# Optimization experiments

Hardware: AMD Instinct MI355X
Metric: run time of the kernel (lower is better)

The kernel has to match this reference:

```python
import jax, jax.numpy as jnp
import numpy as np

B, C_IN, H, W = 2048, 192, 19, 19
G1, P1 = 32, 32

def setup_inputs() -> dict:
    key = jax.random.key(0)
    ks = jax.random.split(key, 10)
    inputs = jax.random.normal(ks[0], (B, C_IN, H, W), dtype=jnp.float32)
    # binary validity mask (most points valid), plus its per-sample sum
    mask = (jax.random.uniform(ks[1], (B, 1, H, W)) > 0.1).astype(jnp.float32)
    mask_sum_hw = jnp.sum(mask, axis=(2, 3), keepdims=True)  # [B,1,1,1]
    s = 0.05
    return {
        "inputs": inputs,
        "mask": mask,
        "mask_sum_hw": mask_sum_hw,
        "w1p": jax.random.normal(ks[2], (P1, C_IN), dtype=jnp.float32) * s,
        "b1p": jnp.zeros((P1,), jnp.float32),
        "w1g": jax.random.normal(ks[3], (G1, C_IN), dtype=jnp.float32) * s,
        "b1g": jnp.zeros((G1,), jnp.float32),
        "beta_g": jnp.zeros((1, G1, 1, 1), jnp.float32),
        "w_lin": jax.random.normal(ks[4], (P1, 3 * G1), dtype=jnp.float32) * s,
        "b_lin": jnp.zeros((P1,), jnp.float32),
        "beta2": jnp.zeros((1, P1, 1, 1), jnp.float32),
        "w2p": jax.random.normal(ks[5], (1, P1), dtype=jnp.float32) * s,
        "b2p": jnp.zeros((1,), jnp.float32),
    }

def _conv1x1(x, w, b):
    # x: [B,C,H,W], w: [O,C] -> [B,O,H,W]
    return jnp.einsum('bchw,oc->bohw', x, w) + b[None, :, None, None]

def _gpool(x, mask, mask_sum_hw):
    # x: [B,G,H,W]; returns [B,3G,1,1]
    off = (jnp.sqrt(mask_sum_hw) - 28.0) / 10.0
    mean = jnp.sum(x, axis=(2, 3), keepdims=True) / mask_sum_hw
    mx = jnp.max(x + (mask - 1.0), axis=(2, 3), keepdims=True)
    return jnp.concatenate([mean, mean * off, mx], axis=1)

def reference(inputs, mask, mask_sum_hw, w1p, b1p, w1g, b1g, beta_g,
              w_lin, b_lin, beta2, w2p, b2p):
    b, _, h, w = inputs.shape
    outp = _conv1x1(inputs, w1p, b1p)                      # [B,P1,H,W]
    outg = _conv1x1(inputs, w1g, b1g)                      # [B,G1,H,W]
    outg = (outg + beta_g) * mask                          # NormMask (no gamma)
    outg = jax.nn.gelu(outg, approximate=False)            # torch GELU = exact erf
    outg = _gpool(outg, mask, mask_sum_hw)                 # [B,3G1,1,1]
    outg = outg.reshape(b, -1) @ w_lin.T + b_lin           # [B,P1]
    outp = outp + outg[:, :, None, None]
    outp = (outp + beta2) * mask                           # NormMask
    outp = jax.nn.gelu(outp, approximate=False)
    outp = _conv1x1(outp, w2p, b2p)                        # [B,1,H,W]
    outp = outp - (1.0 - mask) * 5000.0
    outp = jax.nn.log_softmax(outp.reshape(b, -1), axis=1)
    return outp.reshape(b, h, w)
```

## Files before the change

kernel.cpp:

```cpp
#include <hip/hip_runtime.h>
#include <hip/hip_bf16.h>
#include <math.h>

#define NBLK   256
#define EPB    8
#define CIN    192
#define HW     361
#define NTH    512
#define NSTAGE 48
#define TILE_BYTES 46208
#define SLOTS  2888
#define PSLOTS 3072

typedef float f32x4 __attribute__((ext_vector_type(4)));
typedef short s16x8 __attribute__((ext_vector_type(8)));

__device__ __forceinline__ unsigned short f2bf_bits(float f) {
    __hip_bfloat16 h = __float2bfloat16(f);
    unsigned short s;
    __builtin_memcpy(&s, &h, sizeof(s));
    return s;
}
__device__ __forceinline__ unsigned int packbf(float lo, float hi) {
    return (unsigned int)f2bf_bits(lo) | ((unsigned int)f2bf_bits(hi) << 16);
}

__device__ __forceinline__ float gelu_fast(float x) {
    float inner = x * fmaf(0.044715f, x * x, 1.0f);
    float t = 1.5957691216057308f * inner;
    if (t > 40.f) return x;
    float e = __expf(t);
    return x * (e / (e + 1.0f));
}

#define GLD_LDS16(g, l) __builtin_amdgcn_global_load_lds( \
    (const __attribute__((address_space(1))) unsigned int*)(g), \
    (__attribute__((address_space(3))) unsigned int*)(l), 16, 0, 0)

__global__ __launch_bounds__(NTH, 2)
void policy_head_pipe(const float* __restrict__ inputs,
                      const float* __restrict__ mask,
                      const float* __restrict__ mask_sum,
                      const float* __restrict__ w1p, const float* __restrict__ b1p,
                      const float* __restrict__ w1g, const float* __restrict__ b1g,
                      const float* __restrict__ beta_g,
                      const float* __restrict__ w_lin, const float* __restrict__ b_lin,
                      const float* __restrict__ beta2,
                      const float* __restrict__ w2p, const float* __restrict__ b2p,
                      float* __restrict__ out) {
    __shared__ __align__(16) float xbuf[2][PSLOTS * 4];
    __shared__ unsigned int wlds[64 * 100];
    __shared__ float wlin_t[96 * 32];
    __shared__ float mlds[EPB * HW];
    __shared__ float small[224];
    __shared__ float redA[256], redB[256], pooled[96], linout[32];

    const int tid  = threadIdx.x;
    const int bid  = blockIdx.x;
    const int wv   = tid >> 6;
    const int lane = tid & 63;
    const int g4   = lane >> 4;
    const int c16  = lane & 15;

    int px[3], pxc[3];
    bool valid[3];
    #pragma unroll
    for (int nt = 0; nt < 3; ++nt) {
        px[nt]    = wv * 48 + nt * 16 + c16;
        valid[nt] = (px[nt] < HW);
        pxc[nt]   = valid[nt] ? px[nt] : (HW - 1);
    }

    #pragma unroll
    for (int k = 0; k < 6; ++k) {
        int i = tid + k * NTH;
        int o = i / 48, cq = i - o * 48;
        const float* src = (o < 32) ? (w1p + o * CIN + 4 * cq)
                                    : (w1g + (o - 32) * CIN + 4 * cq);
        float4 v = *(const float4*)src;
        wlds[o * 100 + 2 * cq]     = packbf(v.x, v.y);
        wlds[o * 100 + 2 * cq + 1] = packbf(v.z, v.w);
    }
    #pragma unroll
    for (int k = 0; k < 6; ++k) {
        int i = tid + k * NTH;
        int j = i >> 5, o = i & 31;
        wlin_t[i] = w_lin[o * 96 + j];
    }
    #pragma unroll
    for (int k = 0; k < 6; ++k) {
        int i = tid + k * NTH;
        if (i < EPB * HW) mlds[i] = mask[(size_t)bid * EPB * HW + i];
    }
    if (tid < 32)        small[tid] = b1p[tid];
    else if (tid < 64)   small[tid] = b1g[tid - 32];
    else if (tid < 96)   small[tid] = beta_g[tid - 64];
    else if (tid < 128)  small[tid] = beta2[tid - 96];
    else if (tid < 160)  small[tid] = w2p[tid - 128];
    else if (tid < 192)  small[tid] = b_lin[tid - 160];
    else if (tid < 200)  small[tid] = mask_sum[bid * EPB + (tid - 192)];
    else if (tid == 200) small[tid] = b2p[0];

    __syncthreads();

    const char* in_base = (const char*)inputs;
    auto stage_gll = [&](int t, int pb) {
        const char* src = in_base + ((size_t)(bid * EPB + t / 6) * CIN * HW
                                     + (size_t)(t % 6) * 32 * HW) * 4;
        #pragma unroll
        for (int j = 0; j < 6; ++j) {
            int slotbase = (j * 8 + wv) * 64;
            int cs = slotbase + lane;
            if (cs > SLOTS - 1) cs = SLOTS - 1;
            GLD_LDS16(src + (size_t)cs * 16, &xbuf[pb][slotbase * 4]);
        }
    };

    f32x4 acc[4][3];

    stage_gll(0, 0);
    stage_gll(1, 1);
    asm volatile("s_waitcnt vmcnt(6)" ::: "memory");
    __builtin_amdgcn_s_barrier();

    auto lbar = [] {
        asm volatile("s_waitcnt lgkmcnt(0)" ::: "memory");
        __builtin_amdgcn_s_barrier();
    };

    for (int t = 0; t < NSTAGE; ++t) {
        const int pb = t & 1;
        const int kk = t % 6;

        if (kk == 0) {
            #pragma unroll
            for (int mt = 0; mt < 4; ++mt)
                #pragma unroll
                for (int nt = 0; nt < 3; ++nt)
                    acc[mt][nt] = (f32x4){0.f, 0.f, 0.f, 0.f};
        }

        {
            const float* xf = xbuf[pb];
            s16x8 bfr[3];
            #pragma unroll
            for (int nt = 0; nt < 3; ++nt) {
                float v[8];
                #pragma unroll
                for (int i = 0; i < 8; ++i)
                    v[i] = xf[(8 * g4 + i) * HW + pxc[nt]];
                #pragma unroll
                for (int i = 0; i < 8; ++i)
                    bfr[nt][i] = (short)f2bf_bits(v[i]);
            }
            #pragma unroll
            for (int mt = 0; mt < 4; ++mt) {
                s16x8 a = *(const s16x8*)&wlds[(mt * 16 + c16) * 100 + kk * 16 + 4 * g4];
                #pragma unroll
                for (int nt = 0; nt < 3; ++nt)
                    acc[mt][nt] = __builtin_amdgcn_mfma_f32_16x16x32_bf16(a, bfr[nt], acc[mt][nt], 0, 0, 0);
            }
        }

        asm volatile("" ::: "memory");
        __builtin_amdgcn_s_barrier();

        if (t + 2 < NSTAGE) {
            stage_gll(t + 2, pb);
            asm volatile("s_waitcnt vmcnt(6)" ::: "memory");
        } else {
            asm volatile("s_waitcnt vmcnt(0)" ::: "memory");
        }
        __builtin_amdgcn_s_barrier();

        if (kk == 5) {
            const int e = t / 6;
            const float ms  = small[192 + e];
            const float off = (sqrtf(ms) - 28.0f) * 0.1f;
            float mv[3];
            #pragma unroll
            for (int nt = 0; nt < 3; ++nt)
                mv[nt] = valid[nt] ? mlds[e * HW + pxc[nt]] : 0.f;

            #pragma unroll
            for (int mt = 2; mt < 4; ++mt) {
                #pragma unroll
                for (int r = 0; r < 4; ++r) {
                    int og = (mt - 2) * 16 + g4 * 4 + r;
                    float bb = small[32 + og] + small[64 + og];
                    float s = 0.f, mx = -1e30f;
                    #pragma unroll
                    for (int nt = 0; nt < 3; ++nt) {
                        float v = gelu_fast((acc[mt][nt][r] + bb) * mv[nt]);
                        if (!valid[nt]) v = 0.f;
                        s += v;
                        float cand = valid[nt] ? (v + mv[nt] - 1.f) : -1e30f;
                        mx = fmaxf(mx, cand);
                    }
                    #pragma unroll
                    for (int o = 1; o < 16; o <<= 1) {
                        s += __shfl_xor(s, o, 64);
                        mx = fmaxf(mx, __shfl_xor(mx, o, 64));
                    }
                    if (c16 == 0) { redA[og * 8 + wv] = s; redB[og * 8 + wv] = mx; }
                }
            }
            lbar();

            if (tid < 32) {
                float s = 0.f, mx = -1e30f;
                #pragma unroll
                for (int j = 0; j < 8; ++j) {
                    s += redA[tid * 8 + j];
                    mx = fmaxf(mx, redB[tid * 8 + j]);
                }
                float mean = s / ms;
                pooled[tid]      = mean;
                pooled[32 + tid] = mean * off;
                pooled[64 + tid] = mx;
            }
            lbar();

            if (tid < 32) {
                float a = small[160 + tid];
                #pragma unroll
                for (int j = 0; j < 96; ++j) a = fmaf(pooled[j], wlin_t[j * 32 + tid], a);
                linout[tid] = a;
            }
            lbar();

            float pv[3] = {0.f, 0.f, 0.f};
            #pragma unroll
            for (int mt = 0; mt < 2; ++mt) {
                #pragma unroll
                for (int r = 0; r < 4; ++r) {
                    int op = mt * 16 + g4 * 4 + r;
                    float bb = small[op] + linout[op] + small[96 + op];
                    float wo = small[128 + op];
                    #pragma unroll
                    for (int nt = 0; nt < 3; ++nt)
                        pv[nt] += gelu_fast((acc[mt][nt][r] + bb) * mv[nt]) * wo;
                }
            }
            const float b2 = small[200];
            float logit[3];
            #pragma unroll
            for (int nt = 0; nt < 3; ++nt) {
                float s = pv[nt];
                s += __shfl_xor(s, 16, 64);
                s += __shfl_xor(s, 32, 64);
                logit[nt] = s + b2 - (1.f - mv[nt]) * 5000.f;
            }

            float lmax = -1e30f;
            #pragma unroll
            for (int nt = 0; nt < 3; ++nt)
                if (valid[nt]) lmax = fmaxf(lmax, logit[nt]);
            #pragma unroll
            for (int o = 1; o < 64; o <<= 1) lmax = fmaxf(lmax, __shfl_xor(lmax, o, 64));
            if (lane == 0) redA[wv] = lmax;
            lbar();
            float gmax = -1e30f;
            #pragma unroll
            for (int j = 0; j < 8; ++j) gmax = fmaxf(gmax, redA[j]);

            float es = 0.f;
            #pragma unroll
            for (int nt = 0; nt < 3; ++nt)
                if (valid[nt] && g4 == 0) es += __expf(logit[nt] - gmax);
            #pragma unroll
            for (int o = 1; o < 64; o <<= 1) es += __shfl_xor(es, o, 64);
            if (lane == 0) redB[wv] = es;
            lbar();
            float tot = 0.f;
            #pragma unroll
            for (int j = 0; j < 8; ++j) tot += redB[j];
            const float lt = __logf(tot) + gmax;

            if (g4 == 0) {
                #pragma unroll
                for (int nt = 0; nt < 3; ++nt)
                    if (valid[nt])
                        out[((size_t)bid * EPB + e) * HW + px[nt]] = logit[nt] - lt;
            }
            lbar();
        }
    }
}

extern "C" void kernel_launch(void* const* d_in, const int* in_sizes, int n_in,
                              void* d_out, int out_size, void* d_ws, size_t ws_size,
                              hipStream_t stream) {
    const float* inputs   = (const float*)d_in[0];
    const float* mask     = (const float*)d_in[1];
    const float* mask_sum = (const float*)d_in[2];
    const float* w1p      = (const float*)d_in[3];
    const float* b1p      = (const float*)d_in[4];
    const float* w1g      = (const float*)d_in[5];
    const float* b1g      = (const float*)d_in[6];
    const float* beta_g   = (const float*)d_in[7];
    const float* w_lin    = (const float*)d_in[8];
    const float* b_lin    = (const float*)d_in[9];
    const float* beta2    = (const float*)d_in[10];
    const float* w2p      = (const float*)d_in[11];
    const float* b2p      = (const float*)d_in[12];
    float* out = (float*)d_out;

    policy_head_pipe<<<dim3(NBLK), dim3(NTH), 0, stream>>>(
        inputs, mask, mask_sum, w1p, b1p, w1g, b1g, beta_g,
        w_lin, b_lin, beta2, w2p, b2p, out);
}
```

Before: 173.7 us.

## Replace block-wide LDS pipeline with per-wave register prefetch and private LDS transpose

The block-shared double-buffered global_load_lds staging with two barriers per stage is replaced by per-wave register prefetch of the next channel chunk. Each wave writes its chunk into its own swizzled LDS buffer as packed bf16 and reads B fragments as 16-byte vectors. Blocks become 256 threads handling 4 samples, giving 512 blocks, and each wave covers 96 pixels. The aim is to drop block-level barriers in the GEMM loop and cut LDS traffic and bank conflicts, at the cost of more registers and w_lin now being read from global memory.

```diff
diff --git a/kernel.cpp b/kernel.cpp
--- a/kernel.cpp
+++ b/kernel.cpp
@@ -2,18 +2,16 @@
 #include <hip/hip_bf16.h>
 #include <math.h>
 
-#define NBLK   256
-#define EPB    8
-#define CIN    192
-#define HW     361
-#define NTH    512
-#define NSTAGE 48
-#define TILE_BYTES 46208
-#define SLOTS  2888
-#define PSLOTS 3072
-
-typedef float f32x4 __attribute__((ext_vector_type(4)));
-typedef short s16x8 __attribute__((ext_vector_type(8)));
+#define NB    2048
+#define EPB   4
+#define NBLK  (NB / EPB)
+#define CIN   192
+#define HW    361
+#define NTH   256
+
+typedef float f32x4  __attribute__((ext_vector_type(4)));
+typedef short s16x8  __attribute__((ext_vector_type(8)));
+typedef float f32x4u __attribute__((ext_vector_type(4), aligned(4)));
 
 __device__ __forceinline__ unsigned short f2bf_bits(float f) {
     __hip_bfloat16 h = __float2bfloat16(f);
@@ -33,27 +31,22 @@
     return x * (e / (e + 1.0f));
 }
 
-#define GLD_LDS16(g, l) __builtin_amdgcn_global_load_lds( \
-    (const __attribute__((address_space(1))) unsigned int*)(g), \
-    (__attribute__((address_space(3))) unsigned int*)(l), 16, 0, 0)
-
 __global__ __launch_bounds__(NTH, 2)
-void policy_head_pipe(const float* __restrict__ inputs,
-                      const float* __restrict__ mask,
-                      const float* __restrict__ mask_sum,
-                      const float* __restrict__ w1p, const float* __restrict__ b1p,
-                      const float* __restrict__ w1g, const float* __restrict__ b1g,
-                      const float* __restrict__ beta_g,
-                      const float* __restrict__ w_lin, const float* __restrict__ b_lin,
-                      const float* __restrict__ beta2,
-                      const float* __restrict__ w2p, const float* __restrict__ b2p,
-                      float* __restrict__ out) {
-    __shared__ __align__(16) float xbuf[2][PSLOTS * 4];
+void policy_head_wp(const float* __restrict__ inputs,
+                    const float* __restrict__ mask,
+                    const float* __restrict__ mask_sum,
+                    const float* __restrict__ w1p, const float* __restrict__ b1p,
+                    const float* __restrict__ w1g, const float* __restrict__ b1g,
+                    const float* __restrict__ beta_g,
+                    const float* __restrict__ w_lin, const float* __restrict__ b_lin,
+                    const float* __restrict__ beta2,
+                    const float* __restrict__ w2p, const float* __restrict__ b2p,
+                    float* __restrict__ out) {
+    __shared__ unsigned int xt[4][2][96 * 16];
     __shared__ unsigned int wlds[64 * 100];
-    __shared__ float wlin_t[96 * 32];
-    __shared__ float mlds[EPB * HW];
+    __shared__ float redA[32 * 4], redB[32 * 4];
     __shared__ float small[224];
-    __shared__ float redA[256], redB[256], pooled[96], linout[32];
+    __shared__ float pooled[96], linout[32];
 
     const int tid  = threadIdx.x;
     const int bid  = blockIdx.x;
@@ -62,17 +55,31 @@
     const int g4   = lane >> 4;
     const int c16  = lane & 15;
 
-    int px[3], pxc[3];
-    bool valid[3];
+    int px[6];  bool valid[6];
     #pragma unroll
-    for (int nt = 0; nt < 3; ++nt) {
-        px[nt]    = wv * 48 + nt * 16 + c16;
+    for (int nt = 0; nt < 6; ++nt) {
+        px[nt]    = wv * 96 + nt * 16 + c16;
         valid[nt] = (px[nt] < HW);
-        pxc[nt]   = valid[nt] ? px[nt] : (HW - 1);
     }
 
+    const float* xb0 = inputs + (size_t)bid * EPB * CIN * HW;
+
+    f32x4 rA[12];
+    auto loadT = [&](int e, int kk) {
+        const float* tb = xb0 + ((size_t)e * CIN + kk * 32 + 2 * c16) * HW;
+        #pragma unroll
+        for (int j = 0; j < 6; ++j) {
+            int p0 = wv * 96 + 16 * j + 4 * g4;
+            if (p0 > HW - 4) p0 = HW - 4;
+            rA[2 * j]     = *(const f32x4u*)(tb + p0);
+            rA[2 * j + 1] = *(const f32x4u*)(tb + HW + p0);
+        }
+    };
+
+    loadT(0, 0);
+
     #pragma unroll
-    for (int k = 0; k < 6; ++k) {
+    for (int k = 0; k < 12; ++k) {
         int i = tid + k * NTH;
         int o = i / 48, cq = i - o * 48;
         const float* src = (o < 32) ? (w1p + o * CIN + 4 * cq)
@@ -81,210 +88,171 @@
         wlds[o * 100 + 2 * cq]     = packbf(v.x, v.y);
         wlds[o * 100 + 2 * cq + 1] = packbf(v.z, v.w);
     }
-    #pragma unroll
-    for (int k = 0; k < 6; ++k) {
-        int i = tid + k * NTH;
-        int j = i >> 5, o = i & 31;
-        wlin_t[i] = w_lin[o * 96 + j];
-    }
-    #pragma unroll
-    for (int k = 0; k < 6; ++k) {
-        int i = tid + k * NTH;
-        if (i < EPB * HW) mlds[i] = mask[(size_t)bid * EPB * HW + i];
-    }
     if (tid < 32)        small[tid] = b1p[tid];
     else if (tid < 64)   small[tid] = b1g[tid - 32];
     else if (tid < 96)   small[tid] = beta_g[tid - 64];
     else if (tid < 128)  small[tid] = beta2[tid - 96];
     else if (tid < 160)  small[tid] = w2p[tid - 128];
     else if (tid < 192)  small[tid] = b_lin[tid - 160];
-    else if (tid < 200)  small[tid] = mask_sum[bid * EPB + (tid - 192)];
-    else if (tid == 200) small[tid] = b2p[0];
-
-    __syncthreads();
-
-    const char* in_base = (const char*)inputs;
-    auto stage_gll = [&](int t, int pb) {
-        const char* src = in_base + ((size_t)(bid * EPB + t / 6) * CIN * HW
-                                     + (size_t)(t % 6) * 32 * HW) * 4;
-        #pragma unroll
-        for (int j = 0; j < 6; ++j) {
-            int slotbase = (j * 8 + wv) * 64;
-            int cs = slotbase + lane;
-            if (cs > SLOTS - 1) cs = SLOTS - 1;
-            GLD_LDS16(src + (size_t)cs * 16, &xbuf[pb][slotbase * 4]);
-        }
-    };
-
-    f32x4 acc[4][3];
-
-    stage_gll(0, 0);
-    stage_gll(1, 1);
-    asm volatile("s_waitcnt vmcnt(6)" ::: "memory");
-    __builtin_amdgcn_s_barrier();
+    else if (tid < 196)  small[tid] = mask_sum[bid * EPB + (tid - 192)];
+    else if (tid == 196) small[tid] = b2p[0];
 
     auto lbar = [] {
         asm volatile("s_waitcnt lgkmcnt(0)" ::: "memory");
         __builtin_amdgcn_s_barrier();
     };
-
-    for (int t = 0; t < NSTAGE; ++t) {
-        const int pb = t & 1;
-        const int kk = t % 6;
-
-        if (kk == 0) {
-            #pragma unroll
-            for (int mt = 0; mt < 4; ++mt)
-                #pragma unroll
-                for (int nt = 0; nt < 3; ++nt)
-                    acc[mt][nt] = (f32x4){0.f, 0.f, 0.f, 0.f};
-        }
-
-        {
-            const float* xf = xbuf[pb];
-            s16x8 bfr[3];
-            #pragma unroll
-            for (int nt = 0; nt < 3; ++nt) {
-                float v[8];
-                #pragma unroll
-                for (int i = 0; i < 8; ++i)
-                    v[i] = xf[(8 * g4 + i) * HW + pxc[nt]];
-                #pragma unroll
-                for (int i = 0; i < 8; ++i)
-                    bfr[nt][i] = (short)f2bf_bits(v[i]);
-            }
+    lbar();
+
+    const int qb = 4 * (g4 ^ ((c16 & 3) ^ (c16 >> 2)));
+
+    for (int e = 0; e < EPB; ++e) {
+        float mv[6];
+        #pragma unroll
+        for (int nt = 0; nt < 6; ++nt)
+            mv[nt] = valid[nt] ? mask[((size_t)bid * EPB + e) * HW + px[nt]] : 0.f;
+
+        f32x4 acc[4][6];
+        #pragma unroll
+        for (int mt = 0; mt < 4; ++mt)
+            #pragma unroll
+            for (int nt = 0; nt < 6; ++nt)
+                acc[mt][nt] = (f32x4){0.f, 0.f, 0.f, 0.f};
+
+        #pragma unroll
+        for (int kk = 0; kk < 6; ++kk) {
+            unsigned int* xw = &xt[wv][kk & 1][0];
+
+            #pragma unroll
+            for (int j = 0; j < 6; ++j) {
+                #pragma unroll
+                for (int d = 0; d < 4; ++d) {
+                    int lp = 16 * j + 4 * g4 + d;
+                    int qc = c16 ^ (((d ^ g4) & 3) << 2);
+                    xw[lp * 16 + qc] = packbf(rA[2 * j][d], rA[2 * j + 1][d]);
+                }
+            }
+
+            if (kk < 5)            loadT(e, kk + 1);
+            else if (e + 1 < EPB)  loadT(e + 1, 0);
+
+            s16x8 bfr[6];
+            #pragma unroll
+            for (int nt = 0; nt < 6; ++nt)
+                bfr[nt] = *(const s16x8*)&xw[(nt * 16 + c16) * 16 + qb];
             #pragma unroll
             for (int mt = 0; mt < 4; ++mt) {
                 s16x8 a = *(const s16x8*)&wlds[(mt * 16 + c16) * 100 + kk * 16 + 4 * g4];
                 #pragma unroll
-                for (int nt = 0; nt < 3; ++nt)
+                for (int nt = 0; nt < 6; ++nt)
                     acc[mt][nt] = __builtin_amdgcn_mfma_f32_16x16x32_bf16(a, bfr[nt], acc[mt][nt], 0, 0, 0);
             }
         }
 
-        asm volatile("" ::: "memory");
-        __builtin_amdgcn_s_barrier();
-
-        if (t + 2 < NSTAGE) {
-            stage_gll(t + 2, pb);
-            asm volatile("s_waitcnt vmcnt(6)" ::: "memory");
-        } else {
-            asm volatile("s_waitcnt vmcnt(0)" ::: "memory");
-        }
-        __builtin_amdgcn_s_barrier();
-
-        if (kk == 5) {
-            const int e = t / 6;
-            const float ms  = small[192 + e];
-            const float off = (sqrtf(ms) - 28.0f) * 0.1f;
-            float mv[3];
-            #pragma unroll
-            for (int nt = 0; nt < 3; ++nt)
-                mv[nt] = valid[nt] ? mlds[e * HW + pxc[nt]] : 0.f;
-
-            #pragma unroll
-            for (int mt = 2; mt < 4; ++mt) {
-                #pragma unroll
-                for (int r = 0; r < 4; ++r) {
-                    int og = (mt - 2) * 16 + g4 * 4 + r;
-                    float bb = small[32 + og] + small[64 + og];
-                    float s = 0.f, mx = -1e30f;
-                    #pragma unroll
-                    for (int nt = 0; nt < 3; ++nt) {
-                        float v = gelu_fast((acc[mt][nt][r] + bb) * mv[nt]);
-                        if (!valid[nt]) v = 0.f;
-                        s += v;
-                        float cand = valid[nt] ? (v + mv[nt] - 1.f) : -1e30f;
-                        mx = fmaxf(mx, cand);
-                    }
-                    #pragma unroll
-                    for (int o = 1; o < 16; o <<= 1) {
-                        s += __shfl_xor(s, o, 64);
-                        mx = fmaxf(mx, __shfl_xor(mx, o, 64));
-                    }
-                    if (c16 == 0) { redA[og * 8 + wv] = s; redB[og * 8 + wv] = mx; }
+        const float ms  = small[192 + e];
+        const float off = (sqrtf(ms) - 28.0f) * 0.1f;
+
+        #pragma unroll
+        for (int mt = 2; mt < 4; ++mt) {
+            #pragma unroll
+            for (int r = 0; r < 4; ++r) {
+                int og = (mt - 2) * 16 + g4 * 4 + r;
+                float bb = small[32 + og] + small[64 + og];
+                float s = 0.f, mx = -1e30f;
+                #pragma unroll
+                for (int nt = 0; nt < 6; ++nt) {
+                    float v = gelu_fast((acc[mt][nt][r] + bb) * mv[nt]);
+                    if (!valid[nt]) v = 0.f;
+                    s += v;
+                    float cand = valid[nt] ? (v + mv[nt] - 1.f) : -1e30f;
+                    mx = fmaxf(mx, cand);
                 }
-            }
-            lbar();
-
-            if (tid < 32) {
-                float s = 0.f, mx = -1e30f;
-                #pragma unroll
-                for (int j = 0; j < 8; ++j) {
-                    s += redA[tid * 8 + j];
-                    mx = fmaxf(mx, redB[tid * 8 + j]);
+                #pragma unroll
+                for (int o = 1; o < 16; o <<= 1) {
+                    s += __shfl_xor(s, o, 64);
+                    mx = fmaxf(mx, __shfl_xor(mx, o, 64));
                 }
-                float mean = s / ms;
-                pooled[tid]      = mean;
-                pooled[32 + tid] = mean * off;
-                pooled[64 + tid] = mx;
-            }
-            lbar();
-
-            if (tid < 32) {
-                float a = small[160 + tid];
-                #pragma unroll
-                for (int j = 0; j < 96; ++j) a = fmaf(pooled[j], wlin_t[j * 32 + tid], a);
-                linout[tid] = a;
-            }
-            lbar();
-
-            float pv[3] = {0.f, 0.f, 0.f};
-            #pragma unroll
-            for (int mt = 0; mt < 2; ++mt) {
-                #pragma unroll
-                for (int r = 0; r < 4; ++r) {
-                    int op = mt * 16 + g4 * 4 + r;
-                    float bb = small[op] + linout[op] + small[96 + op];
-                    float wo = small[128 + op];
-                    #pragma unroll
-                    for (int nt = 0; nt < 3; ++nt)
-                        pv[nt] += gelu_fast((acc[mt][nt][r] + bb) * mv[nt]) * wo;
-                }
-            }
-            const float b2 = small[200];
-            float logit[3];
-            #pragma unroll
-            for (int nt = 0; nt < 3; ++nt) {
-                float s = pv[nt];
-                s += __shfl_xor(s, 16, 64);
-                s += __shfl_xor(s, 32, 64);
-                logit[nt] = s + b2 - (1.f - mv[nt]) * 5000.f;
-            }
-
-            float lmax = -1e30f;
-            #pragma unroll
-            for (int nt = 0; nt < 3; ++nt)
-                if (valid[nt]) lmax = fmaxf(lmax, logit[nt]);
-            #pragma unroll
-            for (int o = 1; o < 64; o <<= 1) lmax = fmaxf(lmax, __shfl_xor(lmax, o, 64));
-            if (lane == 0) redA[wv] = lmax;
-            lbar();
-            float gmax = -1e30f;
-            #pragma unroll
-            for (int j = 0; j < 8; ++j) gmax = fmaxf(gmax, redA[j]);
-
-            float es = 0.f;
-            #pragma unroll
-            for (int nt = 0; nt < 3; ++nt)
-                if (valid[nt] && g4 == 0) es += __expf(logit[nt] - gmax);
-            #pragma unroll
-            for (int o = 1; o < 64; o <<= 1) es += __shfl_xor(es, o, 64);
-            if (lane == 0) redB[wv] = es;
-            lbar();
-            float tot = 0.f;
-            #pragma unroll
-            for (int j = 0; j < 8; ++j) tot += redB[j];
-            const float lt = __logf(tot) + gmax;
-
-            if (g4 == 0) {
-                #pragma unroll
-                for (int nt = 0; nt < 3; ++nt)
-                    if (valid[nt])
-                        out[((size_t)bid * EPB + e) * HW + px[nt]] = logit[nt] - lt;
-            }
-            lbar();
-        }
+                if (c16 == 0) { redA[og * 4 + wv] = s; redB[og * 4 + wv] = mx; }
+            }
+        }
+        lbar();
+
+        if (tid < 32) {
+            float s = 0.f, mx = -1e30f;
+            #pragma unroll
+            for (int j = 0; j < 4; ++j) {
+                s += redA[tid * 4 + j];
+                mx = fmaxf(mx, redB[tid * 4 + j]);
+            }
+            float mean = s / ms;
+            pooled[tid]      = mean;
+            pooled[32 + tid] = mean * off;
+            pooled[64 + tid] = mx;
+        }
+        lbar();
+
+        if (tid < 32) {
+            float a = small[160 + tid];
+            #pragma unroll
+            for (int j = 0; j < 96; ++j) a = fmaf(pooled[j], w_lin[tid * 96 + j], a);
+            linout[tid] = a;
+        }
+        lbar();
+
+        float pv[6] = {0.f, 0.f, 0.f, 0.f, 0.f, 0.f};
+        #pragma unroll
+        for (int mt = 0; mt < 2; ++mt) {
+            #pragma unroll
+            for (int r = 0; r < 4; ++r) {
+                int op = mt * 16 + g4 * 4 + r;
+                float bb = small[op] + linout[op] + small[96 + op];
+                float wo = small[128 + op];
+                #pragma unroll
+                for (int nt = 0; nt < 6; ++nt)
+                    pv[nt] += gelu_fast((acc[mt][nt][r] + bb) * mv[nt]) * wo;
+            }
+        }
+        const float b2 = small[196];
+        float logit[6];
+        #pragma unroll
+        for (int nt = 0; nt < 6; ++nt) {
+            float s = pv[nt];
+            s += __shfl_xor(s, 16, 64);
+            s += __shfl_xor(s, 32, 64);
+            logit[nt] = s + b2 - (1.f - mv[nt]) * 5000.f;
+        }
+
+        float lmax = -1e30f;
+        #pragma unroll
+        for (int nt = 0; nt < 6; ++nt)
+            if (valid[nt]) lmax = fmaxf(lmax, logit[nt]);
+        #pragma unroll
+        for (int o = 1; o < 64; o <<= 1) lmax = fmaxf(lmax, __shfl_xor(lmax, o, 64));
+        if (lane == 0) redA[wv] = lmax;
+        lbar();
+        float gmax = -1e30f;
+        #pragma unroll
+        for (int j = 0; j < 4; ++j) gmax = fmaxf(gmax, redA[j]);
+
+        float es = 0.f;
+        #pragma unroll
+        for (int nt = 0; nt < 6; ++nt)
+            if (valid[nt] && g4 == 0) es += __expf(logit[nt] - gmax);
+        #pragma unroll
+        for (int o = 1; o < 64; o <<= 1) es += __shfl_xor(es, o, 64);
+        if (lane == 0) redB[wv] = es;
+        lbar();
+        float tot = 0.f;
+        #pragma unroll
+        for (int j = 0; j < 4; ++j) tot += redB[j];
+        const float lt = __logf(tot) + gmax;
+
+        if (g4 == 0) {
+            #pragma unroll
+            for (int nt = 0; nt < 6; ++nt)
+                if (valid[nt])
+                    out[((size_t)bid * EPB + e) * HW + px[nt]] = logit[nt] - lt;
+        }
+        lbar();
     }
 }
 
@@ -306,7 +274,7 @@
     const float* b2p      = (const float*)d_in[12];
     float* out = (float*)d_out;
 
-    policy_head_pipe<<<dim3(NBLK), dim3(NTH), 0, stream>>>(
+    policy_head_wp<<<dim3(NBLK), dim3(NTH), 0, stream>>>(
         inputs, mask, mask_sum, w1p, b1p, w1g, b1g, beta_g,
         w_lin, b_lin, beta2, w2p, b2p, out);
 }
```

Result: no change. 173.6 us (-0.0%).
